# Performance work log

Measured on AMD Instinct MI355X. Metric: run time of the kernel, lower is better.

Reference implementation:

```python
import jax, jax.numpy as jnp
import numpy as np
from jax.scipy.special import logsumexp

B, T, NT = 8192, 512, 7  # batch, seq_len, num_tags


def setup_inputs() -> dict:
    key = jax.random.key(0)
    k1, k2, k3, k4, k5 = jax.random.split(key, 5)
    emissions = jax.random.normal(k1, (B, T, NT), dtype=jnp.float32)
    labels = jax.random.randint(k2, (B, T), 0, NT)
    mask = jnp.ones((B, T), dtype=jnp.int32)  # first timestep must be on (torchcrf requirement)
    # CRF parameters (torchcrf initializes uniform in [-0.1, 0.1])
    start_transitions = jax.random.uniform(k3, (NT,), minval=-0.1, maxval=0.1, dtype=jnp.float32)
    end_transitions = jax.random.uniform(k4, (NT,), minval=-0.1, maxval=0.1, dtype=jnp.float32)
    transitions = jax.random.uniform(k5, (NT, NT), minval=-0.1, maxval=0.1, dtype=jnp.float32)
    return {
        "emissions": emissions,
        "labels": labels,
        "mask": mask,
        "start_transitions": start_transitions,
        "end_transitions": end_transitions,
        "transitions": transitions,
    }


def _crf_neg_log_likelihood(emissions, labels, mask, start_transitions, end_transitions, transitions):
    # emissions: (B, T, NT); labels: (B, T) int; mask: (B, T) {0,1}
    b, t, nt = emissions.shape
    maskf = mask.astype(emissions.dtype)
    batch_idx = jnp.arange(b)

    # ---- numerator: score of the gold tag path (fully vectorized) ----
    tags = jnp.where(labels < 0, 0, labels)  # labels[labels < 0] = 0 in the torch module
    num = start_transitions[tags[:, 0]] + emissions[batch_idx, 0, tags[:, 0]]
    trans_score = transitions[tags[:, :-1], tags[:, 1:]]                      # (B, T-1)
    emit_score = jnp.take_along_axis(emissions[:, 1:], tags[:, 1:, None], axis=2)[..., 0]  # (B, T-1)
    num = num + jnp.sum((trans_score + emit_score) * maskf[:, 1:], axis=1)
    seq_ends = jnp.sum(mask, axis=1).astype(jnp.int32) - 1                     # (B,)
    last_tags = tags[batch_idx, seq_ends]
    num = num + end_transitions[last_tags]

    # ---- denominator: log partition via forward-algorithm scan over time ----
    init_score = start_transitions[None, :] + emissions[:, 0]  # (B, NT)

    def step(score, inp):
        emit_t, m_t = inp  # (B, NT), (B,)
        # broadcast: score over previous tag, transitions (prev, next), emissions at next tag
        next_score = logsumexp(score[:, :, None] + transitions[None, :, :] + emit_t[:, None, :], axis=1)
        score = jnp.where(m_t[:, None] > 0, next_score, score)
        return score, None

    xs = (jnp.moveaxis(emissions[:, 1:], 1, 0), mask[:, 1:].T)  # (T-1, B, NT), (T-1, B)
    final_score, _ = jax.lax.scan(step, init_score, xs)
    den = logsumexp(final_score + end_transitions[None, :], axis=1)  # (B,)

    # torchcrf default reduction='sum'; module returns loss = -crf(...)
    return jnp.sum(den - num)


def reference(emissions, labels, mask, start_transitions, end_transitions, transitions):
    return _crf_neg_log_likelihood(emissions, labels, mask, start_transitions, end_transitions, transitions)
```

## Files before the change

kernel.cpp:

```cpp
#include <hip/hip_runtime.h>


#define Bsz 8192
#define Tsz 512
#define NTG 7
#define NCH 16
#define CS  32

__device__ __forceinline__ float rfl(float x) {
    return __int_as_float(__builtin_amdgcn_readfirstlane(__float_as_int(x)));
}

__global__ __launch_bounds__(256) void crf_chunk_kernel(
    const float* __restrict__ em, const int* __restrict__ labels,
    const int* __restrict__ mask, const float* __restrict__ startT,
    const float* __restrict__ trans,
    float* __restrict__ Mbuf, float* __restrict__ lsbuf,
    float* __restrict__ numbuf, int* __restrict__ cntbuf)
{
    const int tid = blockIdx.x * blockDim.x + threadIdx.x;
    const int r = tid & (Bsz - 1);
    const int c = tid >> 13;

    __shared__ float transS[NTG * NTG];
    if (threadIdx.x < NTG * NTG) transS[threadIdx.x] = trans[threadIdx.x];
    __syncthreads();

    float W[49];
#pragma unroll
    for (int k = 0; k < 49; ++k) W[k] = rfl(__expf(trans[k]));

    float M[49];
#pragma unroll
    for (int k = 0; k < 49; ++k) M[k] = 0.0f;
#pragma unroll
    for (int i = 0; i < 7; ++i) M[i * 7 + i] = 1.0f;

    float logscale = 0.0f;
    float num = 0.0f;
    int   cnt = 0;

    const int t0 = c * CS;
    const float* emr  = em + (size_t)r * (Tsz * NTG) + (size_t)t0 * NTG;
    const int*   labr = labels + r * Tsz + t0;
    const int*   mskr = mask   + r * Tsz + t0;

    int lprev = 0;
    if (c > 0) { lprev = labr[-1]; if (lprev < 0) lprev = 0; }

#pragma unroll 2
    for (int g = 0; g < CS / 4; ++g) {
        float4 ev[7];
        const float4* ep = (const float4*)(emr + g * (4 * NTG));
#pragma unroll
        for (int q = 0; q < 7; ++q) ev[q] = ep[q];
        const float* eraw = (const float*)&ev[0];

        int4 lab4 = *(const int4*)(labr + g * 4);
        int4 msk4 = *(const int4*)(mskr + g * 4);
        int labs[4] = {lab4.x, lab4.y, lab4.z, lab4.w};
        int msks[4] = {msk4.x, msk4.y, msk4.z, msk4.w};

#pragma unroll
        for (int s = 0; s < 4; ++s) {
            const int t = t0 + g * 4 + s;
            int lc = labs[s]; if (lc < 0) lc = 0;
            const float mf = (float)msks[s];
            cnt += msks[s];

            float esel = eraw[s * 7 + 0];
#pragma unroll
            for (int j = 1; j < 7; ++j) esel = (lc == j) ? eraw[s * 7 + j] : esel;

            if (t == 0) {
                num += startT[lc] + esel;
            } else {
                num += mf * (transS[lprev * 7 + lc] + esel);
                if (msks[s] > 0) {
                    float e[7];
#pragma unroll
                    for (int j = 0; j < 7; ++j) e[j] = __expf(eraw[s * 7 + j]);
#pragma unroll
                    for (int i = 0; i < 7; ++i) {
                        float tmp[7];
#pragma unroll
                        for (int j = 0; j < 7; ++j) tmp[j] = 0.0f;
#pragma unroll
                        for (int k = 0; k < 7; ++k) {
                            const float mik = M[i * 7 + k];
#pragma unroll
                            for (int j = 0; j < 7; ++j)
                                tmp[j] = fmaf(mik, W[k * 7 + j], tmp[j]);
                        }
#pragma unroll
                        for (int j = 0; j < 7; ++j) M[i * 7 + j] = tmp[j] * e[j];
                    }
                }
            }
            lprev = lc;
        }

        if (g & 1) {
            float mx = 1e-30f;
#pragma unroll
            for (int k = 0; k < 49; ++k) mx = fmaxf(mx, M[k]);
            const float inv = 1.0f / mx;
#pragma unroll
            for (int k = 0; k < 49; ++k) M[k] *= inv;
            logscale += __logf(mx);
        }
    }

    float* Mo = Mbuf + (size_t)c * 49 * Bsz + r;
#pragma unroll
    for (int k = 0; k < 49; ++k) Mo[k * Bsz] = M[k];
    lsbuf[c * Bsz + r]  = logscale;
    numbuf[c * Bsz + r] = num;
    cntbuf[c * Bsz + r] = cnt;
}

__global__ __launch_bounds__(256) void crf_combine_kernel(
    const float* __restrict__ em, const int* __restrict__ labels,
    const float* __restrict__ startT, const float* __restrict__ endT,
    const float* __restrict__ Mbuf, const float* __restrict__ lsbuf,
    const float* __restrict__ numbuf, const int* __restrict__ cntbuf,
    float* __restrict__ out)
{
    const int r = blockIdx.x * blockDim.x + threadIdx.x;

    const float* em0 = em + (size_t)r * (Tsz * NTG);
    float v[7];
#pragma unroll
    for (int j = 0; j < 7; ++j) v[j] = __expf(startT[j] + em0[j]);

    float ls = 0.0f, num = 0.0f;
    int cnt = 0;

    for (int c = 0; c < NCH; ++c) {
        const float* Mc = Mbuf + (size_t)c * 49 * Bsz + r;
        float nv[7];
#pragma unroll
        for (int j = 0; j < 7; ++j) nv[j] = 0.0f;
#pragma unroll
        for (int i = 0; i < 7; ++i) {
            const float vi = v[i];
#pragma unroll
            for (int j = 0; j < 7; ++j)
                nv[j] = fmaf(vi, Mc[(i * 7 + j) * Bsz], nv[j]);
        }
        float mx = 1e-30f;
#pragma unroll
        for (int j = 0; j < 7; ++j) mx = fmaxf(mx, nv[j]);
        const float inv = 1.0f / mx;
#pragma unroll
        for (int j = 0; j < 7; ++j) v[j] = nv[j] * inv;
        ls  += __logf(mx) + lsbuf[c * Bsz + r];
        num += numbuf[c * Bsz + r];
        cnt += cntbuf[c * Bsz + r];
    }

    float dsum = 0.0f;
#pragma unroll
    for (int j = 0; j < 7; ++j) dsum += v[j] * __expf(endT[j]);
    const float den = ls + __logf(dsum);

    int se = cnt - 1; if (se < 0) se = 0;
    int lt = labels[r * Tsz + se]; if (lt < 0) lt = 0;
    num += endT[lt];

    float val = den - num;

    __shared__ float red[256];
    red[threadIdx.x] = val;
    __syncthreads();
    for (int off = 128; off > 0; off >>= 1) {
        if (threadIdx.x < off) red[threadIdx.x] += red[threadIdx.x + off];
        __syncthreads();
    }
    if (threadIdx.x == 0) atomicAdd(out, red[0]);
}

extern "C" void kernel_launch(void* const* d_in, const int* in_sizes, int n_in,
                              void* d_out, int out_size, void* d_ws, size_t ws_size,
                              hipStream_t stream) {
    const float* em     = (const float*)d_in[0];
    const int*   labels = (const int*)d_in[1];
    const int*   mask   = (const int*)d_in[2];
    const float* startT = (const float*)d_in[3];
    const float* endT   = (const float*)d_in[4];
    const float* trans  = (const float*)d_in[5];
    float* out = (float*)d_out;

    float* ws     = (float*)d_ws;
    float* Mbuf   = ws;
    float* lsbuf  = Mbuf + (size_t)NCH * 49 * Bsz;
    float* numbuf = lsbuf + (size_t)NCH * Bsz;
    int*   cntbuf = (int*)(numbuf + (size_t)NCH * Bsz);
    (void)in_sizes; (void)n_in; (void)out_size; (void)ws_size;

    hipMemsetAsync(out, 0, sizeof(float), stream);

    crf_chunk_kernel<<<(Bsz * NCH) / 256, 256, 0, stream>>>(
        em, labels, mask, startT, trans, Mbuf, lsbuf, numbuf, cntbuf);
    crf_combine_kernel<<<Bsz / 256, 256, 0, stream>>>(
        em, labels, startT, endT, Mbuf, lsbuf, numbuf, cntbuf, out);
}
```

Before: 274.3 us.

## Fuse chunk and combine stages through LDS with wave-parallel chunk combination

The two-kernel scheme is merged into one kernel. Each block handles 8 rows split into 32 chunks of 16 steps, keeps the per-chunk 7x7 transfer matrices in LDS instead of global workspace, and combines them with wave-level shuffles across 49 lanes. A small reduce kernel replaces the memset and atomic. This removes global Mbuf traffic and a launch. In exchange it uses about 50KB of LDS per block, which limits occupancy, and changes the memory access pattern so adjacent threads now read different chunks of the same row.

New measurement: 272.2 us. No clear change (-0.8%).

```diff
diff --git a/kernel.cpp b/kernel.cpp
--- a/kernel.cpp
+++ b/kernel.cpp
@@ -4,26 +4,50 @@
 #define Bsz 8192
 #define Tsz 512
 #define NTG 7
-#define NCH 16
-#define CS  32
+#define NCH 32
+#define CS  16
+#define RPB 8
+#define THB 256
 
 __device__ __forceinline__ float rfl(float x) {
     return __int_as_float(__builtin_amdgcn_readfirstlane(__float_as_int(x)));
 }
 
-__global__ __launch_bounds__(256) void crf_chunk_kernel(
+__device__ __forceinline__ float wsumf(float x) {
+#pragma unroll
+    for (int m = 1; m < 64; m <<= 1) x += __shfl_xor(x, m, 64);
+    return x;
+}
+__device__ __forceinline__ int wsumi(int x) {
+#pragma unroll
+    for (int m = 1; m < 64; m <<= 1) x += __shfl_xor(x, m, 64);
+    return x;
+}
+__device__ __forceinline__ float wmaxf(float x) {
+#pragma unroll
+    for (int m = 1; m < 64; m <<= 1) x = fmaxf(x, __shfl_xor(x, m, 64));
+    return x;
+}
+
+__global__ __launch_bounds__(THB) void crf_fused_kernel(
     const float* __restrict__ em, const int* __restrict__ labels,
     const int* __restrict__ mask, const float* __restrict__ startT,
-    const float* __restrict__ trans,
-    float* __restrict__ Mbuf, float* __restrict__ lsbuf,
-    float* __restrict__ numbuf, int* __restrict__ cntbuf)
+    const float* __restrict__ endT, const float* __restrict__ trans,
+    float* __restrict__ blockpart)
 {
-    const int tid = blockIdx.x * blockDim.x + threadIdx.x;
-    const int r = tid & (Bsz - 1);
-    const int c = tid >> 13;
-
-    __shared__ float transS[NTG * NTG];
-    if (threadIdx.x < NTG * NTG) transS[threadIdx.x] = trans[threadIdx.x];
+    __shared__ float ldsM[THB * 49 + 20];
+    __shared__ float ldsLs[THB];
+    __shared__ float ldsNum[THB];
+    __shared__ int   ldsCnt[THB];
+    __shared__ float transS[52];
+    __shared__ float rowval[RPB];
+
+    const int t  = threadIdx.x;
+    const int c  = t & (NCH - 1);
+    const int rl = t >> 5;
+    const int r  = blockIdx.x * RPB + rl;
+
+    if (t < 49) transS[t] = trans[t];
     __syncthreads();
 
     float W[49];
@@ -36,9 +60,8 @@
 #pragma unroll
     for (int i = 0; i < 7; ++i) M[i * 7 + i] = 1.0f;
 
-    float logscale = 0.0f;
-    float num = 0.0f;
-    int   cnt = 0;
+    float logscale = 0.0f, num = 0.0f;
+    int cnt = 0;
 
     const int t0 = c * CS;
     const float* emr  = em + (size_t)r * (Tsz * NTG) + (size_t)t0 * NTG;
@@ -48,10 +71,10 @@
     int lprev = 0;
     if (c > 0) { lprev = labr[-1]; if (lprev < 0) lprev = 0; }
 
-#pragma unroll 2
+#pragma unroll
     for (int g = 0; g < CS / 4; ++g) {
         float4 ev[7];
-        const float4* ep = (const float4*)(emr + g * (4 * NTG));
+        const float4* ep = (const float4*)(emr + g * 28);
 #pragma unroll
         for (int q = 0; q < 7; ++q) ev[q] = ep[q];
         const float* eraw = (const float*)&ev[0];
@@ -63,7 +86,7 @@
 
 #pragma unroll
         for (int s = 0; s < 4; ++s) {
-            const int t = t0 + g * 4 + s;
+            const int tt = t0 + g * 4 + s;
             int lc = labs[s]; if (lc < 0) lc = 0;
             const float mf = (float)msks[s];
             cnt += msks[s];
@@ -72,7 +95,7 @@
 #pragma unroll
             for (int j = 1; j < 7; ++j) esel = (lc == j) ? eraw[s * 7 + j] : esel;
 
-            if (t == 0) {
+            if (tt == 0) {
                 num += startT[lc] + esel;
             } else {
                 num += mf * (transS[lprev * 7 + lc] + esel);
@@ -99,7 +122,6 @@
             }
             lprev = lc;
         }
-
         if (g & 1) {
             float mx = 1e-30f;
 #pragma unroll
@@ -111,73 +133,76 @@
         }
     }
 
-    float* Mo = Mbuf + (size_t)c * 49 * Bsz + r;
-#pragma unroll
-    for (int k = 0; k < 49; ++k) Mo[k * Bsz] = M[k];
-    lsbuf[c * Bsz + r]  = logscale;
-    numbuf[c * Bsz + r] = num;
-    cntbuf[c * Bsz + r] = cnt;
-}
-
-__global__ __launch_bounds__(256) void crf_combine_kernel(
-    const float* __restrict__ em, const int* __restrict__ labels,
-    const float* __restrict__ startT, const float* __restrict__ endT,
-    const float* __restrict__ Mbuf, const float* __restrict__ lsbuf,
-    const float* __restrict__ numbuf, const int* __restrict__ cntbuf,
-    float* __restrict__ out)
+#pragma unroll
+    for (int k = 0; k < 49; ++k) ldsM[t * 49 + k] = M[k];
+    ldsLs[t]  = logscale;
+    ldsNum[t] = num;
+    ldsCnt[t] = cnt;
+    __syncthreads();
+
+    const int lane = t & 63;
+    const int wv   = t >> 6;
+    const int idiv = lane / 7;
+
+    for (int rr = 0; rr < 2; ++rr) {
+        const int rl2 = wv * 2 + rr;
+        const int r2  = blockIdx.x * RPB + rl2;
+
+        float v = 0.0f;
+        if (lane < 7) v = __expf(startT[lane] + em[(size_t)r2 * (Tsz * NTG) + lane]);
+        float ls = 0.0f;
+
+        for (int cc = 0; cc < NCH; ++cc) {
+            const float Mk = ldsM[(rl2 * NCH + cc) * 49 + lane];
+            const float vi = __shfl(v, idiv, 64);
+            float p = (lane < 49) ? vi * Mk : 0.0f;
+            p += __shfl_down(p, 28, 64);
+            p += __shfl_down(p, 14, 64);
+            p += __shfl_down(p, 7, 64);
+            const float mx = wmaxf(p);
+            v = p * (1.0f / mx);
+            ls += __logf(mx);
+        }
+
+        float lsA  = (lane < NCH) ? ldsLs[rl2 * NCH + lane]  : 0.0f;
+        float numA = (lane < NCH) ? ldsNum[rl2 * NCH + lane] : 0.0f;
+        int   cntA = (lane < NCH) ? ldsCnt[rl2 * NCH + lane] : 0;
+        ls += wsumf(lsA);
+        float numt = wsumf(numA);
+        int   cntt = wsumi(cntA);
+
+        float term = (lane < 7) ? v * __expf(endT[lane]) : 0.0f;
+        const float den = ls + __logf(wsumf(term));
+
+        int se = cntt - 1; if (se < 0) se = 0;
+        int lt = labels[r2 * Tsz + se]; if (lt < 0) lt = 0;
+        numt += endT[lt];
+
+        if (lane == 0) rowval[rl2] = den - numt;
+    }
+    __syncthreads();
+
+    if (t == 0) {
+        float s = 0.0f;
+#pragma unroll
+        for (int k = 0; k < RPB; ++k) s += rowval[k];
+        blockpart[blockIdx.x] = s;
+    }
+}
+
+__global__ __launch_bounds__(256) void crf_reduce_kernel(
+    const float* __restrict__ part, float* __restrict__ out)
 {
-    const int r = blockIdx.x * blockDim.x + threadIdx.x;
-
-    const float* em0 = em + (size_t)r * (Tsz * NTG);
-    float v[7];
-#pragma unroll
-    for (int j = 0; j < 7; ++j) v[j] = __expf(startT[j] + em0[j]);
-
-    float ls = 0.0f, num = 0.0f;
-    int cnt = 0;
-
-    for (int c = 0; c < NCH; ++c) {
-        const float* Mc = Mbuf + (size_t)c * 49 * Bsz + r;
-        float nv[7];
-#pragma unroll
-        for (int j = 0; j < 7; ++j) nv[j] = 0.0f;
-#pragma unroll
-        for (int i = 0; i < 7; ++i) {
-            const float vi = v[i];
-#pragma unroll
-            for (int j = 0; j < 7; ++j)
-                nv[j] = fmaf(vi, Mc[(i * 7 + j) * Bsz], nv[j]);
-        }
-        float mx = 1e-30f;
-#pragma unroll
-        for (int j = 0; j < 7; ++j) mx = fmaxf(mx, nv[j]);
-        const float inv = 1.0f / mx;
-#pragma unroll
-        for (int j = 0; j < 7; ++j) v[j] = nv[j] * inv;
-        ls  += __logf(mx) + lsbuf[c * Bsz + r];
-        num += numbuf[c * Bsz + r];
-        cnt += cntbuf[c * Bsz + r];
-    }
-
-    float dsum = 0.0f;
-#pragma unroll
-    for (int j = 0; j < 7; ++j) dsum += v[j] * __expf(endT[j]);
-    const float den = ls + __logf(dsum);
-
-    int se = cnt - 1; if (se < 0) se = 0;
-    int lt = labels[r * Tsz + se]; if (lt < 0) lt = 0;
-    num += endT[lt];
-
-    float val = den - num;
-
+    const int t = threadIdx.x;
+    float s = part[t] + part[t + 256] + part[t + 512] + part[t + 768];
     __shared__ float red[256];
-    red[threadIdx.x] = val;
+    red[t] = s;
     __syncthreads();
     for (int off = 128; off > 0; off >>= 1) {
-        if (threadIdx.x < off) red[threadIdx.x] += red[threadIdx.x + off];
+        if (t < off) red[t] += red[t + off];
         __syncthreads();
     }
-    if (threadIdx.x == 0) atomicAdd(out, red[0]);
+    if (t == 0) out[0] = red[0];
 }
 
 extern "C" void kernel_launch(void* const* d_in, const int* in_sizes, int n_in,
@@ -190,18 +215,10 @@
     const float* endT   = (const float*)d_in[4];
     const float* trans  = (const float*)d_in[5];
     float* out = (float*)d_out;
-
-    float* ws     = (float*)d_ws;
-    float* Mbuf   = ws;
-    float* lsbuf  = Mbuf + (size_t)NCH * 49 * Bsz;
-    float* numbuf = lsbuf + (size_t)NCH * Bsz;
-    int*   cntbuf = (int*)(numbuf + (size_t)NCH * Bsz);
+    float* blockpart = (float*)d_ws;
     (void)in_sizes; (void)n_in; (void)out_size; (void)ws_size;
 
-    hipMemsetAsync(out, 0, sizeof(float), stream);
-
-    crf_chunk_kernel<<<(Bsz * NCH) / 256, 256, 0, stream>>>(
-        em, labels, mask, startT, trans, Mbuf, lsbuf, numbuf, cntbuf);
-    crf_combine_kernel<<<Bsz / 256, 256, 0, stream>>>(
-        em, labels, startT, endT, Mbuf, lsbuf, numbuf, cntbuf, out);
-}
+    crf_fused_kernel<<<Bsz / RPB, THB, 0, stream>>>(
+        em, labels, mask, startT, endT, trans, blockpart);
+    crf_reduce_kernel<<<1, 256, 0, stream>>>(blockpart, out);
+}
```

## Double chunk count, interleave chunks per row, store fp16 partial matrices

Applied to the files above, without the earlier changes.

Raises the number of time chunks from 16 to 32, halving each chunk to 16 steps. Remaps threads so adjacent lanes handle consecutive chunks of the same sequence rather than the same chunk of consecutive sequences. The partial transfer matrices are stored in half precision to cut workspace traffic. The combine kernel now uses 64-thread blocks, double-buffers the chunk matrix loads, and replaces the shared-memory reduction with wave shuffles. The risks are uncoalesced emission reads, because lanes now stride across time, and precision loss from fp16 storage of the normalized matrices.

Measured after the change: 582.9 us. 112% more time.

```diff
diff --git a/kernel.cpp b/kernel.cpp
--- a/kernel.cpp
+++ b/kernel.cpp
@@ -1,29 +1,30 @@
 #include <hip/hip_runtime.h>
+#include <hip/hip_fp16.h>
 
 
 #define Bsz 8192
 #define Tsz 512
 #define NTG 7
-#define NCH 16
-#define CS  32
+#define NCH 32
+#define CS  16
 
 __device__ __forceinline__ float rfl(float x) {
     return __int_as_float(__builtin_amdgcn_readfirstlane(__float_as_int(x)));
 }
 
-__global__ __launch_bounds__(256) void crf_chunk_kernel(
+__global__ __launch_bounds__(256, 4) void crf_op_kernel(
     const float* __restrict__ em, const int* __restrict__ labels,
     const int* __restrict__ mask, const float* __restrict__ startT,
     const float* __restrict__ trans,
-    float* __restrict__ Mbuf, float* __restrict__ lsbuf,
+    __half* __restrict__ Mh, float* __restrict__ lsbuf,
     float* __restrict__ numbuf, int* __restrict__ cntbuf)
 {
     const int tid = blockIdx.x * blockDim.x + threadIdx.x;
-    const int r = tid & (Bsz - 1);
-    const int c = tid >> 13;
-
-    __shared__ float transS[NTG * NTG];
-    if (threadIdx.x < NTG * NTG) transS[threadIdx.x] = trans[threadIdx.x];
+    const int c = tid & (NCH - 1);
+    const int r = tid >> 5;
+
+    __shared__ float transS[49];
+    if (threadIdx.x < 49) transS[threadIdx.x] = trans[threadIdx.x];
     __syncthreads();
 
     float W[49];
@@ -36,9 +37,8 @@
 #pragma unroll
     for (int i = 0; i < 7; ++i) M[i * 7 + i] = 1.0f;
 
-    float logscale = 0.0f;
-    float num = 0.0f;
-    int   cnt = 0;
+    float logscale = 0.0f, num = 0.0f;
+    int cnt = 0;
 
     const int t0 = c * CS;
     const float* emr  = em + (size_t)r * (Tsz * NTG) + (size_t)t0 * NTG;
@@ -48,14 +48,16 @@
     int lprev = 0;
     if (c > 0) { lprev = labr[-1]; if (lprev < 0) lprev = 0; }
 
-#pragma unroll 2
+#pragma unroll
     for (int g = 0; g < CS / 4; ++g) {
-        float4 ev[7];
-        const float4* ep = (const float4*)(emr + g * (4 * NTG));
-#pragma unroll
-        for (int q = 0; q < 7; ++q) ev[q] = ep[q];
-        const float* eraw = (const float*)&ev[0];
-
+        float er[28];
+        const float4* ep = (const float4*)(emr + g * 28);
+#pragma unroll
+        for (int q = 0; q < 7; ++q) {
+            float4 v = ep[q];
+            er[4 * q + 0] = v.x; er[4 * q + 1] = v.y;
+            er[4 * q + 2] = v.z; er[4 * q + 3] = v.w;
+        }
         int4 lab4 = *(const int4*)(labr + g * 4);
         int4 msk4 = *(const int4*)(mskr + g * 4);
         int labs[4] = {lab4.x, lab4.y, lab4.z, lab4.w};
@@ -63,23 +65,23 @@
 
 #pragma unroll
         for (int s = 0; s < 4; ++s) {
-            const int t = t0 + g * 4 + s;
+            const int tt = t0 + g * 4 + s;
             int lc = labs[s]; if (lc < 0) lc = 0;
             const float mf = (float)msks[s];
             cnt += msks[s];
 
-            float esel = eraw[s * 7 + 0];
-#pragma unroll
-            for (int j = 1; j < 7; ++j) esel = (lc == j) ? eraw[s * 7 + j] : esel;
-
-            if (t == 0) {
+            float esel = er[s * 7 + 0];
+#pragma unroll
+            for (int j = 1; j < 7; ++j) esel = (lc == j) ? er[s * 7 + j] : esel;
+
+            if (tt == 0) {
                 num += startT[lc] + esel;
             } else {
                 num += mf * (transS[lprev * 7 + lc] + esel);
                 if (msks[s] > 0) {
                     float e[7];
 #pragma unroll
-                    for (int j = 0; j < 7; ++j) e[j] = __expf(eraw[s * 7 + j]);
+                    for (int j = 0; j < 7; ++j) e[j] = __expf(er[s * 7 + j]);
 #pragma unroll
                     for (int i = 0; i < 7; ++i) {
                         float tmp[7];
@@ -99,7 +101,6 @@
             }
             lprev = lc;
         }
-
         if (g & 1) {
             float mx = 1e-30f;
 #pragma unroll
@@ -111,57 +112,74 @@
         }
     }
 
-    float* Mo = Mbuf + (size_t)c * 49 * Bsz + r;
-#pragma unroll
-    for (int k = 0; k < 49; ++k) Mo[k * Bsz] = M[k];
+#pragma unroll
+    for (int k = 0; k < 49; ++k)
+        Mh[((size_t)c * 49 + k) * Bsz + r] = __float2half(M[k]);
     lsbuf[c * Bsz + r]  = logscale;
     numbuf[c * Bsz + r] = num;
     cntbuf[c * Bsz + r] = cnt;
 }
 
-__global__ __launch_bounds__(256) void crf_combine_kernel(
+__global__ __launch_bounds__(64, 1) void crf_chain_kernel(
     const float* __restrict__ em, const int* __restrict__ labels,
     const float* __restrict__ startT, const float* __restrict__ endT,
-    const float* __restrict__ Mbuf, const float* __restrict__ lsbuf,
+    const __half* __restrict__ Mh, const float* __restrict__ lsbuf,
     const float* __restrict__ numbuf, const int* __restrict__ cntbuf,
     float* __restrict__ out)
 {
-    const int r = blockIdx.x * blockDim.x + threadIdx.x;
-
-    const float* em0 = em + (size_t)r * (Tsz * NTG);
-    float v[7];
-#pragma unroll
-    for (int j = 0; j < 7; ++j) v[j] = __expf(startT[j] + em0[j]);
+    const int r = blockIdx.x * 64 + threadIdx.x;
+
+    float va[7];
+#pragma unroll
+    for (int j = 0; j < 7; ++j)
+        va[j] = __expf(startT[j] + em[(size_t)r * (Tsz * NTG) + j]);
 
     float ls = 0.0f, num = 0.0f;
     int cnt = 0;
 
-    for (int c = 0; c < NCH; ++c) {
-        const float* Mc = Mbuf + (size_t)c * 49 * Bsz + r;
-        float nv[7];
-#pragma unroll
-        for (int j = 0; j < 7; ++j) nv[j] = 0.0f;
-#pragma unroll
-        for (int i = 0; i < 7; ++i) {
-            const float vi = v[i];
-#pragma unroll
-            for (int j = 0; j < 7; ++j)
-                nv[j] = fmaf(vi, Mc[(i * 7 + j) * Bsz], nv[j]);
-        }
-        float mx = 1e-30f;
-#pragma unroll
-        for (int j = 0; j < 7; ++j) mx = fmaxf(mx, nv[j]);
-        const float inv = 1.0f / mx;
-#pragma unroll
-        for (int j = 0; j < 7; ++j) v[j] = nv[j] * inv;
-        ls  += __logf(mx) + lsbuf[c * Bsz + r];
-        num += numbuf[c * Bsz + r];
-        cnt += cntbuf[c * Bsz + r];
+    float bufA[49], bufB[49];
+
+#define LOADC(buf, cc) {                                                   \
+    const int _c = (cc);                                                   \
+    _Pragma("unroll")                                                      \
+    for (int k = 0; k < 49; ++k)                                           \
+        buf[k] = __half2float(Mh[((size_t)_c * 49 + k) * Bsz + r]);        \
+    ls  += lsbuf[_c * Bsz + r];                                            \
+    num += numbuf[_c * Bsz + r];                                           \
+    cnt += cntbuf[_c * Bsz + r]; }
+
+#define STEP(buf) {                                                        \
+    float nv[7];                                                           \
+    _Pragma("unroll")                                                      \
+    for (int j = 0; j < 7; ++j) nv[j] = 0.0f;                              \
+    _Pragma("unroll")                                                      \
+    for (int i = 0; i < 7; ++i) {                                          \
+        const float vi = va[i];                                            \
+        _Pragma("unroll")                                                  \
+        for (int j = 0; j < 7; ++j)                                        \
+            nv[j] = fmaf(vi, buf[i * 7 + j], nv[j]);                       \
+    }                                                                      \
+    float mx = 1e-30f;                                                     \
+    _Pragma("unroll")                                                      \
+    for (int j = 0; j < 7; ++j) mx = fmaxf(mx, nv[j]);                     \
+    const float inv = 1.0f / mx;                                           \
+    _Pragma("unroll")                                                      \
+    for (int j = 0; j < 7; ++j) va[j] = nv[j] * inv;                       \
+    ls += __logf(mx); }
+
+    LOADC(bufA, 0);
+    for (int p = 0; p < NCH / 2; ++p) {
+        LOADC(bufB, 2 * p + 1);
+        STEP(bufA);
+        if (p < NCH / 2 - 1) LOADC(bufA, 2 * p + 2);
+        STEP(bufB);
     }
+#undef LOADC
+#undef STEP
 
     float dsum = 0.0f;
 #pragma unroll
-    for (int j = 0; j < 7; ++j) dsum += v[j] * __expf(endT[j]);
+    for (int j = 0; j < 7; ++j) dsum += va[j] * __expf(endT[j]);
     const float den = ls + __logf(dsum);
 
     int se = cnt - 1; if (se < 0) se = 0;
@@ -169,15 +187,9 @@
     num += endT[lt];
 
     float val = den - num;
-
-    __shared__ float red[256];
-    red[threadIdx.x] = val;
-    __syncthreads();
-    for (int off = 128; off > 0; off >>= 1) {
-        if (threadIdx.x < off) red[threadIdx.x] += red[threadIdx.x + off];
-        __syncthreads();
-    }
-    if (threadIdx.x == 0) atomicAdd(out, red[0]);
+#pragma unroll
+    for (int m = 1; m < 64; m <<= 1) val += __shfl_xor(val, m, 64);
+    if (threadIdx.x == 0) atomicAdd(out, val);
 }
 
 extern "C" void kernel_launch(void* const* d_in, const int* in_sizes, int n_in,
@@ -191,17 +203,16 @@
     const float* trans  = (const float*)d_in[5];
     float* out = (float*)d_out;
 
-    float* ws     = (float*)d_ws;
-    float* Mbuf   = ws;
-    float* lsbuf  = Mbuf + (size_t)NCH * 49 * Bsz;
-    float* numbuf = lsbuf + (size_t)NCH * Bsz;
-    int*   cntbuf = (int*)(numbuf + (size_t)NCH * Bsz);
+    __half* Mh    = (__half*)d_ws;
+    float*  lsbuf = (float*)(Mh + (size_t)NCH * 49 * Bsz);
+    float*  numbuf = lsbuf + (size_t)NCH * Bsz;
+    int*    cntbuf = (int*)(numbuf + (size_t)NCH * Bsz);
     (void)in_sizes; (void)n_in; (void)out_size; (void)ws_size;
 
     hipMemsetAsync(out, 0, sizeof(float), stream);
 
-    crf_chunk_kernel<<<(Bsz * NCH) / 256, 256, 0, stream>>>(
-        em, labels, mask, startT, trans, Mbuf, lsbuf, numbuf, cntbuf);
-    crf_combine_kernel<<<Bsz / 256, 256, 0, stream>>>(
-        em, labels, startT, endT, Mbuf, lsbuf, numbuf, cntbuf, out);
-}
+    crf_op_kernel<<<(Bsz * NCH) / 256, 256, 0, stream>>>(
+        em, labels, mask, startT, trans, Mh, lsbuf, numbuf, cntbuf);
+    crf_chain_kernel<<<Bsz / 64, 64, 0, stream>>>(
+        em, labels, startT, endT, Mh, lsbuf, numbuf, cntbuf, out);
+}
```
